# Optimization experiments

Measured on AMD Instinct MI355X. Metric: run time of the kernel, lower is better.

Reference implementation:

```python
import jax, jax.numpy as jnp
import numpy as np

N_NODES = 100000
N_EDGES = 3200000
N_GRAPHS = 256
VOCAB = 1500


def gcn_conv(x, edge_index, W, b, n_nodes):
    # x: [N, Fin], edge_index: [2, E] (row=source, col=target)
    h = x @ W  # [N, Fout]
    loops = jnp.arange(n_nodes, dtype=edge_index.dtype)
    row = jnp.concatenate([edge_index[0], loops])
    col = jnp.concatenate([edge_index[1], loops])
    # symmetric normalization with self-loops (PyG GCNConv default)
    deg = jax.ops.segment_sum(jnp.ones_like(col, dtype=h.dtype), col,
                              num_segments=n_nodes)
    dinv = jnp.where(deg > 0, jax.lax.rsqrt(deg), 0.0)
    norm = dinv[row] * dinv[col]  # [E+N]
    msg = h[row] * norm[:, None]  # gather + scale
    out = jax.ops.segment_sum(msg, col, num_segments=n_nodes)  # scatter-add
    return out + b


def setup_inputs() -> dict:
    key = jax.random.key(0)
    k = jax.random.split(key, 8)
    x_ids = jax.random.randint(k[0], (N_NODES,), 0, VOCAB)
    edge_index = jax.random.randint(k[1], (2, N_EDGES), 0, N_NODES)
    batch = jnp.sort(jax.random.randint(k[2], (N_NODES,), 0, N_GRAPHS))
    emb_table = jax.random.normal(k[3], (VOCAB, 16), dtype=jnp.float32)
    W1 = jax.random.normal(k[4], (16, 32), dtype=jnp.float32) * (1.0 / np.sqrt(16))
    b1 = jnp.zeros((32,), dtype=jnp.float32)
    W2 = jax.random.normal(k[5], (32, 41), dtype=jnp.float32) * (1.0 / np.sqrt(32))
    b2 = jnp.zeros((41,), dtype=jnp.float32)
    return {"x_ids": x_ids, "edge_index": edge_index, "batch": batch,
            "emb_table": emb_table, "W1": W1, "b1": b1, "W2": W2, "b2": b2}


def reference(x_ids, edge_index, batch, emb_table, W1, b1, W2, b2):
    x = emb_table[x_ids]                      # embedding lookup [N,16]
    x = gcn_conv(x, edge_index, W1, b1, N_NODES)
    x = jax.nn.relu(x)                        # dropout is identity in eval
    x = gcn_conv(x, edge_index, W2, b2, N_NODES)
    # scatter_add pooling over graphs in batch
    return jax.ops.segment_sum(x, batch, num_segments=N_GRAPHS)  # [G,41]
```

## Files before the change

kernel.cpp:

```cpp
#include <hip/hip_runtime.h>


constexpr int EPB = 16384;
constexpr int BSH = 8;
constexpr int BKTN = 1 << BSH;
constexpr int CAP = 10240;
constexpr int CAPC = 8704;
constexpr int CAPF = 5376;

__device__ inline unsigned short f2bf(float x) {
  unsigned u = __float_as_uint(x);
  u += 0x7FFF + ((u >> 16) & 1);
  return (unsigned short)(u >> 16);
}
__device__ inline float bf2f(unsigned short h) {
  return __uint_as_float((unsigned)h << 16);
}
__device__ inline unsigned pk(float a, float b) {
  return (unsigned)f2bf(a) | ((unsigned)f2bf(b) << 16);
}
__device__ __forceinline__ void add8(float* acc, uint4 v) {
  acc[0] += bf2f(v.x & 0xFFFF); acc[1] += bf2f(v.x >> 16);
  acc[2] += bf2f(v.y & 0xFFFF); acc[3] += bf2f(v.y >> 16);
  acc[4] += bf2f(v.z & 0xFFFF); acc[5] += bf2f(v.z >> 16);
  acc[6] += bf2f(v.w & 0xFFFF); acc[7] += bf2f(v.w >> 16);
}

__device__ __forceinline__ void gather8(const unsigned short* __restrict__ base,
                                        const int* list, int st, int dg,
                                        float acc[8]) {
  int j = 0;
  if (dg >= 8) {
    int r0 = list[st], r1 = list[st + 1], r2 = list[st + 2], r3 = list[st + 3];
    uint4 v0 = *(const uint4*)(base + (size_t)r0 * 16);
    uint4 v1 = *(const uint4*)(base + (size_t)r1 * 16);
    uint4 v2 = *(const uint4*)(base + (size_t)r2 * 16);
    uint4 v3 = *(const uint4*)(base + (size_t)r3 * 16);
    for (j = 4; j + 4 <= dg; j += 4) {
      int s0 = list[st + j], s1 = list[st + j + 1];
      int s2 = list[st + j + 2], s3 = list[st + j + 3];
      uint4 w0 = *(const uint4*)(base + (size_t)s0 * 16);
      uint4 w1 = *(const uint4*)(base + (size_t)s1 * 16);
      uint4 w2 = *(const uint4*)(base + (size_t)s2 * 16);
      uint4 w3 = *(const uint4*)(base + (size_t)s3 * 16);
      add8(acc, v0); add8(acc, v1); add8(acc, v2); add8(acc, v3);
      v0 = w0; v1 = w1; v2 = w2; v3 = w3;
    }
    add8(acc, v0); add8(acc, v1); add8(acc, v2); add8(acc, v3);
  }
  for (; j < dg; ++j)
    add8(acc, *(const uint4*)(base + (size_t)list[st + j] * 16));
}

__device__ __forceinline__ void gather16(const unsigned short* __restrict__ base,
                                         const int* list, int st, int dg,
                                         float acc[16]) {
  int j = 0;
  if (dg >= 4) {
    int r0 = list[st], r1 = list[st + 1];
    uint4 a0 = *(const uint4*)(base + (size_t)r0 * 32);
    uint4 a1 = *(const uint4*)(base + (size_t)r0 * 32 + 8);
    uint4 b0 = *(const uint4*)(base + (size_t)r1 * 32);
    uint4 b1 = *(const uint4*)(base + (size_t)r1 * 32 + 8);
    for (j = 2; j + 2 <= dg; j += 2) {
      int s0 = list[st + j], s1 = list[st + j + 1];
      uint4 c0 = *(const uint4*)(base + (size_t)s0 * 32);
      uint4 c1 = *(const uint4*)(base + (size_t)s0 * 32 + 8);
      uint4 d0 = *(const uint4*)(base + (size_t)s1 * 32);
      uint4 d1 = *(const uint4*)(base + (size_t)s1 * 32 + 8);
      add8(acc, a0); add8(acc + 8, a1);
      add8(acc, b0); add8(acc + 8, b1);
      a0 = c0; a1 = c1; b0 = d0; b1 = d1;
    }
    add8(acc, a0); add8(acc + 8, a1);
    add8(acc, b0); add8(acc + 8, b1);
  }
  for (; j < dg; ++j) {
    int r = list[st + j];
    uint4 v0 = *(const uint4*)(base + (size_t)r * 32);
    uint4 v1 = *(const uint4*)(base + (size_t)r * 32 + 8);
    add8(acc, v0); add8(acc + 8, v1);
  }
}

__device__ __forceinline__ void copy_window(int* list, const int* __restrict__ src,
                                            int n, int tid) {
  const int4* s4 = (const int4*)src;
  int4* d4 = (int4*)list;
  int n4 = n >> 2;
  for (int i = tid; i < n4; i += 512) d4[i] = s4[i];
  for (int i = (n4 << 2) + tid; i < n; i += 512) list[i] = src[i];
}

__device__ __forceinline__ int swz(int b, int nblkp) {
  return (b & 7) * (nblkp >> 3) + (b >> 3);
}

__global__ __launch_bounds__(1024) void k_scatter(const int* __restrict__ row,
                                                  const int* __restrict__ col, int E,
                                                  int nbkt, int nblkp,
                                                  int* __restrict__ cursor,
                                                  int* __restrict__ staging) {
  __shared__ int sbuf[EPB];
  __shared__ int cnt[512], sc[512], cur[512], gbase[512];
  int tid = threadIdx.x;
  int lane = tid & 63, wv = tid >> 6;
  int blk = swz(blockIdx.x, nblkp);
  if (tid < 512) cnt[tid] = 0;
  __syncthreads();
  int e0 = blk * EPB, e1 = min(E, e0 + EPB);
  for (int e = e0 + tid; e < e1; e += 1024)
    atomicAdd(&cnt[col[e] >> BSH], 1);
  __syncthreads();
  if (tid < 512) {
    int c = cnt[tid];
    sc[tid] = c;
    gbase[tid] = c ? atomicAdd(&cursor[tid], c) : 0;
  }
  __syncthreads();
  for (int o = 1; o < 512; o <<= 1) {
    int u = (tid < 512 && tid >= o) ? sc[tid - o] : 0;
    __syncthreads();
    if (tid < 512) sc[tid] += u;
    __syncthreads();
  }
  if (tid < 512) { int st = sc[tid] - cnt[tid]; sc[tid] = st; cur[tid] = st; }
  __syncthreads();
  for (int e = e0 + tid; e < e1; e += 1024) {
    int c = col[e];
    int b = c >> BSH;
    int pos = atomicAdd(&cur[b], 1);
    sbuf[pos] = (row[e] << BSH) | (c & (BKTN - 1));
  }
  __syncthreads();
  for (int b = wv; b < nbkt; b += 16) {
    int lbeg = sc[b], lcnt = cnt[b];
    int gb = gbase[b];
    int lim = CAP - gb;
    if (lcnt > lim) lcnt = lim > 0 ? lim : 0;
    int g = b * CAP + gb;
    for (int j = lane; j < lcnt; j += 64)
      staging[g + j] = sbuf[lbeg + j];
  }
}

__global__ __launch_bounds__(512) void k_build(const int* __restrict__ staging,
                                               const int* __restrict__ cursor,
                                               const int* __restrict__ x_ids,
                                               const float* __restrict__ emb,
                                               int N, int Nh, int nbkt,
                                               int* __restrict__ cp0,
                                               int* __restrict__ cp1,
                                               int* __restrict__ endp,
                                               float* __restrict__ dinv,
                                               unsigned short* __restrict__ ag1,
                                               int* __restrict__ edge_row) {
  __shared__ int list[CAP];
  __shared__ int cnt[512], sc[512], lcur[512];
  int tid = threadIdx.x, b = blockIdx.x;
  int beg = b * CAP;
  int total = min(cursor[b], CAP);
  int end = beg + total;
  cnt[tid] = 0;
  __syncthreads();
  for (int i = beg + tid; i < end; i += 512) {
    int p = staging[i];
    int key = ((p >> BSH) >= Nh ? 256 : 0) | (p & (BKTN - 1));
    atomicAdd(&cnt[key], 1);
  }
  __syncthreads();
  sc[tid] = cnt[tid];
  __syncthreads();
  for (int o = 1; o < 512; o <<= 1) {
    int u = (tid >= o) ? sc[tid - o] : 0;
    __syncthreads();
    sc[tid] += u;
    __syncthreads();
  }
  {
    int excl = sc[tid] - cnt[tid];
    sc[tid] = excl;
    lcur[tid] = excl;
    if (tid < 256) cp0[(b << BSH) + tid] = beg + excl;
    else cp1[(b << BSH) + tid - 256] = beg + excl;
  }
  if (tid == 0) endp[b] = end;
  __syncthreads();
  for (int i = beg + tid; i < end; i += 512) {
    int p = staging[i];
    int key = ((p >> BSH) >= Nh ? 256 : 0) | (p & (BKTN - 1));
    list[atomicAdd(&lcur[key], 1)] = p >> BSH;
  }
  __syncthreads();
  for (int i = beg + tid; i < end; i += 512)
    edge_row[i] = list[i - beg];
  int nloc = tid >> 1, half = tid & 1;
  int node = (b << BSH) + nloc;
  if (node < N) {
    int deg = cnt[nloc] + cnt[256 + nloc];
    float d = rsqrtf((float)(deg + 1));
    if (half == 0) dinv[node] = d;
    const float* er = emb + (size_t)x_ids[node] * 16 + half * 8;
    float4 e0 = *(const float4*)(er);
    float4 e1 = *(const float4*)(er + 4);
    uint4 o;
    o.x = pk(e0.x * d, e0.y * d); o.y = pk(e0.z * d, e0.w * d);
    o.z = pk(e1.x * d, e1.y * d); o.w = pk(e1.z * d, e1.w * d);
    *(uint4*)(ag1 + (size_t)node * 16 + half * 8) = o;
  }
}

__global__ __launch_bounds__(512) void k_fuse1(const unsigned short* __restrict__ ag1,
                                               const int* __restrict__ edge_row,
                                               const int* __restrict__ cp0,
                                               const int* __restrict__ cp1,
                                               const int* __restrict__ endp,
                                               const float* __restrict__ dinv,
                                               const float* __restrict__ W1,
                                               const float* __restrict__ b1, int N,
                                               unsigned short* __restrict__ y1) {
  __shared__ int list[CAPC];
  __shared__ float W[512];
  __shared__ float bb[32];
  int tid = threadIdx.x, b = blockIdx.x;
  W[tid] = W1[tid];
  if (tid < 32) bb[tid] = b1[tid];
  int nloc = tid >> 1, half = tid & 1;
  int node = (b << BSH) + nloc;
  bool valid = node < N;
  int beg = b * CAP;
  int end = endp[b];
  int h1beg = cp1[b << BSH];
  int s0 = 0, e0 = 0, s1 = 0, e1 = 0;
  float acc[8];
  if (valid) {
    s0 = cp0[node];
    e0 = (nloc == BKTN - 1) ? h1beg : cp0[node + 1];
    s1 = cp1[node];
    e1 = (nloc == BKTN - 1) ? end : cp1[node + 1];
    uint4 v = *(const uint4*)(ag1 + (size_t)node * 16 + half * 8);
    acc[0] = bf2f(v.x & 0xFFFF); acc[1] = bf2f(v.x >> 16);
    acc[2] = bf2f(v.y & 0xFFFF); acc[3] = bf2f(v.y >> 16);
    acc[4] = bf2f(v.z & 0xFFFF); acc[5] = bf2f(v.z >> 16);
    acc[6] = bf2f(v.w & 0xFFFF); acc[7] = bf2f(v.w >> 16);
  } else {
#pragma unroll
    for (int k = 0; k < 8; ++k) acc[k] = 0.f;
  }
  for (int cbeg = beg; cbeg < end; cbeg += CAPC) {
    int cend = min(end, cbeg + CAPC);
    __syncthreads();
    copy_window(list, edge_row + cbeg, cend - cbeg, tid);
    __syncthreads();
    if (valid) {
      int st = max(s0, cbeg), en = min(e0, cend);
      if (en > st) gather8(ag1 + half * 8, list, st - cbeg, en - st, acc);
      st = max(s1, cbeg); en = min(e1, cend);
      if (en > st) gather8(ag1 + half * 8, list, st - cbeg, en - st, acc);
    }
  }
  if (!valid) return;
  float d = dinv[node];
  float sx[8], xo[8];
#pragma unroll
  for (int k = 0; k < 8; ++k) sx[k] = acc[k] * d;
#pragma unroll
  for (int k = 0; k < 8; ++k) xo[k] = __shfl_xor(sx[k], 1);
  float x[16];
  if (half == 0) {
#pragma unroll
    for (int k = 0; k < 8; ++k) { x[k] = sx[k]; x[8 + k] = xo[k]; }
  } else {
#pragma unroll
    for (int k = 0; k < 8; ++k) { x[k] = xo[k]; x[8 + k] = sx[k]; }
  }
  int j0 = half * 16;
  float a[16];
#pragma unroll
  for (int j = 0; j < 16; ++j) a[j] = bb[j0 + j];
#pragma unroll
  for (int k = 0; k < 16; ++k) {
    float xv = x[k];
#pragma unroll
    for (int j = 0; j < 16; ++j) a[j] += xv * W[k * 32 + j0 + j];
  }
#pragma unroll
  for (int j = 0; j < 16; ++j) a[j] = fmaxf(a[j], 0.f) * d;
  uint4 o0 = {pk(a[0], a[1]), pk(a[2], a[3]), pk(a[4], a[5]), pk(a[6], a[7])};
  uint4 o1 = {pk(a[8], a[9]), pk(a[10], a[11]), pk(a[12], a[13]), pk(a[14], a[15])};
  unsigned short* yp = y1 + (size_t)node * 32 + half * 16;
  *(uint4*)(yp) = o0;
  *(uint4*)(yp + 8) = o1;
}

__global__ __launch_bounds__(512) void k_fuse2(const unsigned short* __restrict__ y1,
                                               const int* __restrict__ edge_row,
                                               const int* __restrict__ cp0,
                                               const int* __restrict__ cp1,
                                               const int* __restrict__ endp,
                                               const float* __restrict__ dinv,
                                               const int* __restrict__ batch,
                                               int N, int Nh, int nbkt,
                                               float* __restrict__ P) {
  __shared__ int list[CAPF];
  __shared__ float pool[8 * 32];
  int bx = blockIdx.x;
  int hs = (bx >> 2) & 1;
  int b = (bx >> 3) * 4 + (bx & 3);
  if (b >= nbkt) return;
  int tid = threadIdx.x;
  int nloc = tid >> 1, half = tid & 1;
  int node = (b << BSH) + nloc;
  bool valid = node < N;
  int end = endp[b];
  int h1beg = cp1[b << BSH];
  int rbeg = hs ? h1beg : b * CAP;
  int rend = hs ? end : h1beg;
  int ms = 0, me = 0;
  float acc[16];
  if (valid) {
    if (hs == 0) {
      ms = cp0[node];
      me = (nloc == BKTN - 1) ? h1beg : cp0[node + 1];
    } else {
      ms = cp1[node];
      me = (nloc == BKTN - 1) ? end : cp1[node + 1];
    }
  }
  if (valid && ((node >= Nh) ? 1 : 0) == hs) {
    const unsigned short* sp = y1 + (size_t)node * 32 + half * 16;
    uint4 v0 = *(const uint4*)(sp);
    uint4 v1 = *(const uint4*)(sp + 8);
#pragma unroll
    for (int k = 0; k < 16; ++k) acc[k] = 0.f;
    add8(acc, v0); add8(acc + 8, v1);
  } else {
#pragma unroll
    for (int k = 0; k < 16; ++k) acc[k] = 0.f;
  }
  for (int cbeg = rbeg; cbeg < rend; cbeg += CAPF) {
    int cend = min(rend, cbeg + CAPF);
    __syncthreads();
    copy_window(list, edge_row + cbeg, cend - cbeg, tid);
    __syncthreads();
    if (valid) {
      int st = max(ms, cbeg), en = min(me, cend);
      if (en > st) gather16(y1 + half * 16, list, st - cbeg, en - st, acc);
    }
  }
  int myg = -1;
  if (valid) {
    float d = dinv[node];
#pragma unroll
    for (int k = 0; k < 16; ++k) acc[k] *= d;
    myg = batch[node];
  }
  int g0 = batch[b << BSH];
  int g1 = batch[min((b << BSH) + BKTN - 1, N - 1)];
  int pofs = half << 4;
  for (int clo = g0; clo <= g1; clo += 8) {
    for (int j = tid; j < 8 * 32; j += 512) pool[j] = 0.f;
    __syncthreads();
    if (myg >= clo && myg < clo + 8) {
      float* pp = pool + (myg - clo) * 32 + pofs;
#pragma unroll
      for (int k = 0; k < 16; ++k) atomicAdd(pp + k, acc[k]);
    }
    __syncthreads();
    int ng = min(8, g1 - clo + 1);
    for (int j = tid; j < ng * 32; j += 512)
      atomicAdd(&P[(size_t)(clo + (j >> 5)) * 32 + (j & 31)], pool[j]);
    __syncthreads();
  }
}

__global__ __launch_bounds__(64) void k_final(const float* __restrict__ P,
                                              const int* __restrict__ batch, int N,
                                              const float* __restrict__ W2,
                                              const float* __restrict__ b2,
                                              float* __restrict__ out) {
  __shared__ float pr[32];
  __shared__ int se[2];
  int g = blockIdx.x, tid = threadIdx.x;
  if (tid < 2) {
    int v = g + tid;
    int lo = 0, hi = N;
    while (lo < hi) {
      int mid = (lo + hi) >> 1;
      if (batch[mid] < v) lo = mid + 1; else hi = mid;
    }
    se[tid] = lo;
  }
  if (tid < 32) pr[tid] = P[(size_t)g * 32 + tid];
  __syncthreads();
  if (tid < 41) {
    float o = (float)(se[1] - se[0]) * b2[tid];
#pragma unroll
    for (int k = 0; k < 32; ++k) o += pr[k] * W2[k * 41 + tid];
    out[(size_t)g * 41 + tid] = o;
  }
}

extern "C" void kernel_launch(void* const* d_in, const int* in_sizes, int n_in,
                              void* d_out, int out_size, void* d_ws, size_t ws_size,
                              hipStream_t stream) {
  const int* x_ids = (const int*)d_in[0];
  const int* edge_index = (const int*)d_in[1];
  const int* batch = (const int*)d_in[2];
  const float* emb = (const float*)d_in[3];
  const float* W1 = (const float*)d_in[4];
  const float* b1 = (const float*)d_in[5];
  const float* W2 = (const float*)d_in[6];
  const float* b2 = (const float*)d_in[7];
  float* out = (float*)d_out;

  const int N = in_sizes[0];
  const int E = in_sizes[1] / 2;
  const int G = out_size / 41;
  const int Nh = N / 2;
  const int* row = edge_index;
  const int* col = edge_index + E;

  const int nbkt = (N + BKTN - 1) >> BSH;
  int nblk = (E + EPB - 1) / EPB;
  const int nblkp = (nblk + 7) & ~7;
  const int nbkt4 = (nbkt + 3) & ~3;

  char* ws = (char*)d_ws;
  size_t woff = 0;
  auto alloc = [&](size_t bytes) -> char* {
    char* p = ws + woff;
    woff += (bytes + 255) & ~(size_t)255;
    return p;
  };
  int* staging = (int*)alloc((size_t)nbkt * CAP * 4);
  int* edge_row = (int*)alloc((size_t)nbkt * CAP * 4);
  int* cp0 = (int*)alloc((size_t)nbkt * BKTN * 4);
  int* cp1 = (int*)alloc((size_t)nbkt * BKTN * 4);
  float* dinv = (float*)alloc((size_t)N * 4);
  unsigned short* ag1 = (unsigned short*)alloc((size_t)N * 16 * 2);
  unsigned short* y1 = (unsigned short*)alloc((size_t)N * 32 * 2);
  int* endp = (int*)alloc((size_t)nbkt * 4);
  float* P = (float*)alloc((size_t)G * 32 * 4 + (size_t)nbkt * 4);
  int* cursor = (int*)(P + (size_t)G * 32);
  (void)ws_size; (void)n_in;

  hipMemsetAsync(P, 0, (size_t)G * 32 * 4 + (size_t)nbkt * 4, stream);

  k_scatter<<<nblkp, 1024, 0, stream>>>(row, col, E, nbkt, nblkp, cursor, staging);
  k_build<<<nbkt, 512, 0, stream>>>(staging, cursor, x_ids, emb, N, Nh, nbkt,
                                    cp0, cp1, endp, dinv, ag1, edge_row);
  k_fuse1<<<nbkt, 512, 0, stream>>>(ag1, edge_row, cp0, cp1, endp, dinv, W1, b1,
                                    N, y1);
  k_fuse2<<<2 * nbkt4, 512, 0, stream>>>(y1, edge_row, cp0, cp1, endp, dinv,
                                         batch, N, Nh, nbkt, P);
  k_final<<<G, 64, 0, stream>>>(P, batch, N, W2, b2, out);
}
```

Measured before the change: 219.6 us.

## Split fuse2 work into quarter-feature threads over half-buckets

The second aggregation kernel now assigns four threads per node, each gathering 8 bf16 features, instead of two threads handling 16 each. Each block covers half a bucket (128 nodes), so twice as many blocks are launched and every block must reload the bucket's edge window into shared memory. The gather unrolls four neighbours with one 16-byte load each, which lowers per-thread register pressure and exposes more memory-level parallelism. In exchange, the edge list is read twice per bucket and there are more pooling atomics per block.

```diff
diff --git a/kernel.cpp b/kernel.cpp
--- a/kernel.cpp
+++ b/kernel.cpp
@@ -52,35 +52,30 @@
     add8(acc, *(const uint4*)(base + (size_t)list[st + j] * 16));
 }
 
-__device__ __forceinline__ void gather16(const unsigned short* __restrict__ base,
-                                         const int* list, int st, int dg,
-                                         float acc[16]) {
+__device__ __forceinline__ void gather_quad(const unsigned short* __restrict__ base,
+                                            const int* list, int st, int dg,
+                                            float acc[8]) {
   int j = 0;
-  if (dg >= 4) {
-    int r0 = list[st], r1 = list[st + 1];
-    uint4 a0 = *(const uint4*)(base + (size_t)r0 * 32);
-    uint4 a1 = *(const uint4*)(base + (size_t)r0 * 32 + 8);
-    uint4 b0 = *(const uint4*)(base + (size_t)r1 * 32);
-    uint4 b1 = *(const uint4*)(base + (size_t)r1 * 32 + 8);
-    for (j = 2; j + 2 <= dg; j += 2) {
+  if (dg >= 8) {
+    int r0 = list[st], r1 = list[st + 1], r2 = list[st + 2], r3 = list[st + 3];
+    uint4 v0 = *(const uint4*)(base + (size_t)r0 * 32);
+    uint4 v1 = *(const uint4*)(base + (size_t)r1 * 32);
+    uint4 v2 = *(const uint4*)(base + (size_t)r2 * 32);
+    uint4 v3 = *(const uint4*)(base + (size_t)r3 * 32);
+    for (j = 4; j + 4 <= dg; j += 4) {
       int s0 = list[st + j], s1 = list[st + j + 1];
-      uint4 c0 = *(const uint4*)(base + (size_t)s0 * 32);
-      uint4 c1 = *(const uint4*)(base + (size_t)s0 * 32 + 8);
-      uint4 d0 = *(const uint4*)(base + (size_t)s1 * 32);
-      uint4 d1 = *(const uint4*)(base + (size_t)s1 * 32 + 8);
-      add8(acc, a0); add8(acc + 8, a1);
-      add8(acc, b0); add8(acc + 8, b1);
-      a0 = c0; a1 = c1; b0 = d0; b1 = d1;
-    }
-    add8(acc, a0); add8(acc + 8, a1);
-    add8(acc, b0); add8(acc + 8, b1);
-  }
-  for (; j < dg; ++j) {
-    int r = list[st + j];
-    uint4 v0 = *(const uint4*)(base + (size_t)r * 32);
-    uint4 v1 = *(const uint4*)(base + (size_t)r * 32 + 8);
-    add8(acc, v0); add8(acc + 8, v1);
-  }
+      int s2 = list[st + j + 2], s3 = list[st + j + 3];
+      uint4 w0 = *(const uint4*)(base + (size_t)s0 * 32);
+      uint4 w1 = *(const uint4*)(base + (size_t)s1 * 32);
+      uint4 w2 = *(const uint4*)(base + (size_t)s2 * 32);
+      uint4 w3 = *(const uint4*)(base + (size_t)s3 * 32);
+      add8(acc, v0); add8(acc, v1); add8(acc, v2); add8(acc, v3);
+      v0 = w0; v1 = w1; v2 = w2; v3 = w3;
+    }
+    add8(acc, v0); add8(acc, v1); add8(acc, v2); add8(acc, v3);
+  }
+  for (; j < dg; ++j)
+    add8(acc, *(const uint4*)(base + (size_t)list[st + j] * 32));
 }
 
 __device__ __forceinline__ void copy_window(int* list, const int* __restrict__ src,
@@ -305,11 +300,12 @@
   __shared__ int list[CAPF];
   __shared__ float pool[8 * 32];
   int bx = blockIdx.x;
+  int nh = bx & 1;
   int hs = (bx >> 2) & 1;
-  int b = (bx >> 3) * 4 + (bx & 3);
+  int b = (bx >> 3) * 2 + ((bx >> 1) & 1);
   if (b >= nbkt) return;
   int tid = threadIdx.x;
-  int nloc = tid >> 1, half = tid & 1;
+  int nloc = nh * 128 + (tid >> 2), qf = tid & 3;
   int node = (b << BSH) + nloc;
   bool valid = node < N;
   int end = endp[b];
@@ -317,7 +313,7 @@
   int rbeg = hs ? h1beg : b * CAP;
   int rend = hs ? end : h1beg;
   int ms = 0, me = 0;
-  float acc[16];
+  float acc[8];
   if (valid) {
     if (hs == 0) {
       ms = cp0[node];
@@ -328,15 +324,14 @@
     }
   }
   if (valid && ((node >= Nh) ? 1 : 0) == hs) {
-    const unsigned short* sp = y1 + (size_t)node * 32 + half * 16;
-    uint4 v0 = *(const uint4*)(sp);
-    uint4 v1 = *(const uint4*)(sp + 8);
-#pragma unroll
-    for (int k = 0; k < 16; ++k) acc[k] = 0.f;
-    add8(acc, v0); add8(acc + 8, v1);
+    uint4 v = *(const uint4*)(y1 + (size_t)node * 32 + qf * 8);
+    acc[0] = bf2f(v.x & 0xFFFF); acc[1] = bf2f(v.x >> 16);
+    acc[2] = bf2f(v.y & 0xFFFF); acc[3] = bf2f(v.y >> 16);
+    acc[4] = bf2f(v.z & 0xFFFF); acc[5] = bf2f(v.z >> 16);
+    acc[6] = bf2f(v.w & 0xFFFF); acc[7] = bf2f(v.w >> 16);
   } else {
 #pragma unroll
-    for (int k = 0; k < 16; ++k) acc[k] = 0.f;
+    for (int k = 0; k < 8; ++k) acc[k] = 0.f;
   }
   for (int cbeg = rbeg; cbeg < rend; cbeg += CAPF) {
     int cend = min(rend, cbeg + CAPF);
@@ -345,26 +340,26 @@
     __syncthreads();
     if (valid) {
       int st = max(ms, cbeg), en = min(me, cend);
-      if (en > st) gather16(y1 + half * 16, list, st - cbeg, en - st, acc);
+      if (en > st) gather_quad(y1 + qf * 8, list, st - cbeg, en - st, acc);
     }
   }
   int myg = -1;
   if (valid) {
     float d = dinv[node];
 #pragma unroll
-    for (int k = 0; k < 16; ++k) acc[k] *= d;
+    for (int k = 0; k < 8; ++k) acc[k] *= d;
     myg = batch[node];
   }
-  int g0 = batch[b << BSH];
-  int g1 = batch[min((b << BSH) + BKTN - 1, N - 1)];
-  int pofs = half << 4;
+  int base0 = (b << BSH) + nh * 128;
+  int g0 = batch[min(base0, N - 1)];
+  int g1 = batch[min(base0 + 127, N - 1)];
   for (int clo = g0; clo <= g1; clo += 8) {
     for (int j = tid; j < 8 * 32; j += 512) pool[j] = 0.f;
     __syncthreads();
     if (myg >= clo && myg < clo + 8) {
-      float* pp = pool + (myg - clo) * 32 + pofs;
-#pragma unroll
-      for (int k = 0; k < 16; ++k) atomicAdd(pp + k, acc[k]);
+      float* pp = pool + (myg - clo) * 32 + qf * 8;
+#pragma unroll
+      for (int k = 0; k < 8; ++k) atomicAdd(pp + k, acc[k]);
     }
     __syncthreads();
     int ng = min(8, g1 - clo + 1);
@@ -424,7 +419,7 @@
   const int nbkt = (N + BKTN - 1) >> BSH;
   int nblk = (E + EPB - 1) / EPB;
   const int nblkp = (nblk + 7) & ~7;
-  const int nbkt4 = (nbkt + 3) & ~3;
+  const int nbkt2 = (nbkt + 1) & ~1;
 
   char* ws = (char*)d_ws;
   size_t woff = 0;
@@ -452,7 +447,7 @@
                                     cp0, cp1, endp, dinv, ag1, edge_row);
   k_fuse1<<<nbkt, 512, 0, stream>>>(ag1, edge_row, cp0, cp1, endp, dinv, W1, b1,
                                     N, y1);
-  k_fuse2<<<2 * nbkt4, 512, 0, stream>>>(y1, edge_row, cp0, cp1, endp, dinv,
+  k_fuse2<<<4 * nbkt2, 512, 0, stream>>>(y1, edge_row, cp0, cp1, endp, dinv,
                                          batch, N, Nh, nbkt, P);
   k_final<<<G, 64, 0, stream>>>(P, batch, N, W2, b2, out);
 }
```

Measured after the change: 211.1 us. 3.9% less time.
